# Kernel tuning notes

Measured on AMD Instinct MI355X. Metric: run time of the kernel, lower is better.

Reference implementation:

```python
import jax, jax.numpy as jnp
import numpy as np

N = 50000   # nodes
E = 800000  # edges (avg degree 16)
D = 64      # feature dim (input_dim == hidden_dim == output_dim for num_layer=2)
BN_EPS = 1e-5


def setup_inputs() -> dict:
    key = jax.random.key(0)
    ks = jax.random.split(key, 8)
    def lin_w(k, fan_in, fan_out):
        return jax.random.normal(k, (fan_in, fan_out), jnp.float32) / np.sqrt(fan_in).astype(np.float32)
    inp = {
        "x": jax.random.normal(ks[0], (N, D), jnp.float32),
        "edge_index": jax.random.randint(ks[1], (2, E), 0, N),
    }
    ki = 2
    for l in range(2):
        for s in ("a", "b"):
            inp[f"w{l}{s}"] = lin_w(ks[ki], D, D)
            inp[f"b{l}{s}"] = jnp.zeros((D,), jnp.float32)
            inp[f"g{l}{s}"] = jnp.ones((D,), jnp.float32)   # BN gamma
            inp[f"be{l}{s}"] = jnp.zeros((D,), jnp.float32)  # BN beta
            ki += 1
    inp["lin_w"] = lin_w(ks[6], 2 * D, D)  # JK cat of 2 layers -> 2D, final lin -> D
    inp["lin_b"] = jnp.zeros((D,), jnp.float32)
    return inp


def _bn(h, g, b):
    # BatchNorm1d in training mode: batch statistics over the node axis
    m = h.mean(axis=0)
    v = h.var(axis=0)
    return (h - m) * jax.lax.rsqrt(v + BN_EPS) * g + b


def _gin(h, src, dst, w1, b1, g1, be1, w2, b2, g2, be2):
    # GINConv with eps=0: (1+eps)*x_i + sum_{j->i} x_j, then MLP(Lin-BN-ReLU-Lin-BN-ReLU)
    agg = jax.ops.segment_sum(h[src], dst, num_segments=N) + h
    h = jax.nn.relu(_bn(agg @ w1 + b1, g1, be1))
    return jax.nn.relu(_bn(h @ w2 + b2, g2, be2))


def reference(x, edge_index, w0a, b0a, g0a, be0a, w0b, b0b, g0b, be0b,
              w1a, b1a, g1a, be1a, w1b, b1b, g1b, be1b, lin_w, lin_b):
    src, dst = edge_index[0], edge_index[1]
    h1 = _gin(x, src, dst, w0a, b0a, g0a, be0a, w0b, b0b, g0b, be0b)
    h2 = _gin(h1, src, dst, w1a, b1a, g1a, be1a, w1b, b1b, g1b, be1b)
    # JumpingKnowledge 'cat' over the conv outputs (res[1:]), then final linear
    return jnp.concatenate([h1, h2], axis=1) @ lin_w + lin_b
```

## Files before the change

kernel.cpp:

```cpp
#include <hip/hip_runtime.h>
#include <hip/hip_bf16.h>

#define NN 50000
#define NE 800000
#define BN_EPS 1e-5f
#define CHUNK 4096
#define NCH 196
#define NBK 196

typedef __attribute__((ext_vector_type(4))) float f32x4;
typedef __attribute__((ext_vector_type(8))) short s16x8;
typedef __attribute__((ext_vector_type(4))) short s16x4;

__device__ __forceinline__ float bf2f(__hip_bfloat16 v) { return __bfloat162float(v); }
__device__ __forceinline__ short f2bs(float v) {
    __hip_bfloat16 b = __float2bfloat16(v);
    return __builtin_bit_cast(short, b);
}

__global__ void prep_k(const int* __restrict__ dst, int* __restrict__ part,
                       const float* __restrict__ x, __hip_bfloat16* __restrict__ Xb,
                       const float* __restrict__ w0a, const float* __restrict__ w0b,
                       const float* __restrict__ w1a, const float* __restrict__ w1b,
                       const float* __restrict__ lw,
                       short* __restrict__ Wt0a, short* __restrict__ Wt0b,
                       short* __restrict__ Wt1a, short* __restrict__ Wt1b,
                       short* __restrict__ Wtf) {
    int b = blockIdx.x, t = threadIdx.x;
    if (b < NCH) {
        __shared__ int c[256];
        c[t] = 0;
        __syncthreads();
        int base = b * CHUNK;
        int n = NE - base; if (n > CHUNK) n = CHUNK;
        for (int i = t; i < n; i += 256) atomicAdd(&c[dst[base + i] >> 8], 1);
        __syncthreads();
        part[b * 256 + t] = c[t];
    } else if (b < 196 + 3125) {
        int i = (b - 196) * 256 + t;
        if (i < NN * 16) {
            f32x4 v = *(const f32x4*)(x + (size_t)i * 4);
            s16x4 ov;
            #pragma unroll
            for (int j = 0; j < 4; j++) ov[j] = f2bs(v[j]);
            *(s16x4*)((short*)Xb + (size_t)i * 4) = ov;
        }
    } else {
        int wb = b - 3321;
        if (wb < 4) {
            const float* W = wb == 0 ? w0a : wb == 1 ? w0b : wb == 2 ? w1a : w1b;
            short* Wt = wb == 0 ? Wt0a : wb == 1 ? Wt0b : wb == 2 ? Wt1a : Wt1b;
            for (int e = t; e < 4096; e += 256) {
                int k = e >> 6, n = e & 63;
                Wt[n * 64 + k] = f2bs(W[e]);
            }
        } else {
            for (int e = t; e < 8192; e += 256) {
                int k = e >> 6, n = e & 63;
                Wtf[n * 128 + k] = f2bs(lw[e]);
            }
        }
    }
}

__global__ void bscan_k(const int* __restrict__ part, int* __restrict__ bbase,
                        int* __restrict__ bres, int* __restrict__ off,
                        float* __restrict__ sums) {
    __shared__ int s[256];
    int t = threadIdx.x;
    int v = 0;
    for (int c = 0; c < NCH; c++) v += part[c * 256 + t];
    s[t] = v;
    __syncthreads();
    for (int d = 1; d < 256; d <<= 1) {
        int u = (t >= d) ? s[t - d] : 0;
        __syncthreads();
        s[t] += u;
        __syncthreads();
    }
    int ex = s[t] - v;
    bbase[t] = ex;
    bres[t] = ex;
    if (t == 0) { bbase[256] = NE; off[NN] = NE; }
    sums[t] = 0.f; sums[256 + t] = 0.f;
}

__global__ void bscatter_k(const int* __restrict__ src, const int* __restrict__ dst,
                           int* __restrict__ bres, int* __restrict__ ebuf) {
    __shared__ int cnt[256], loff[256], lcur[256], gst[256], sc[256];
    __shared__ int packed[CHUNK];
    int t = threadIdx.x;
    cnt[t] = 0;
    __syncthreads();
    int base = blockIdx.x * CHUNK;
    int n = NE - base; if (n > CHUNK) n = CHUNK;
    for (int i = t; i < n; i += 256) atomicAdd(&cnt[dst[base + i] >> 8], 1);
    __syncthreads();
    sc[t] = cnt[t];
    __syncthreads();
    for (int d = 1; d < 256; d <<= 1) {
        int u = (t >= d) ? sc[t - d] : 0;
        __syncthreads();
        sc[t] += u;
        __syncthreads();
    }
    loff[t] = sc[t] - cnt[t];
    lcur[t] = loff[t];
    __syncthreads();
    for (int i = t; i < n; i += 256) {
        int d = dst[base + i];
        int b = d >> 8;
        int p = atomicAdd(&lcur[b], 1);
        packed[p] = src[base + i] | ((d & 255) << 16) | (b << 24);
    }
    __syncthreads();
    if (cnt[t]) gst[t] = atomicAdd(&bres[t], cnt[t]);
    __syncthreads();
    for (int i = t; i < n; i += 256) {
        int v = packed[i];
        int b = (v >> 24) & 255;
        ebuf[gst[b] + i - loff[b]] = v & 0xFFFFFF;
    }
}

__global__ void csr_k(const int* __restrict__ bbase, const int* __restrict__ ebuf,
                      int* __restrict__ off, int* __restrict__ adj) {
    __shared__ int cnt[256], loff[256], lcur[256], sc[256];
    int b = blockIdx.x, t = threadIdx.x;
    int s0 = bbase[b], s1 = bbase[b + 1];
    int n = s1 - s0;
    cnt[t] = 0;
    __syncthreads();
    for (int i = t; i < n; i += 256) atomicAdd(&cnt[(ebuf[s0 + i] >> 16) & 255], 1);
    __syncthreads();
    sc[t] = cnt[t];
    __syncthreads();
    for (int d = 1; d < 256; d <<= 1) {
        int u = (t >= d) ? sc[t - d] : 0;
        __syncthreads();
        sc[t] += u;
        __syncthreads();
    }
    loff[t] = sc[t] - cnt[t];
    lcur[t] = loff[t];
    int node = b * 256 + t;
    if (node < NN) off[node] = s0 + loff[t];
    __syncthreads();
    for (int i = t; i < n; i += 256) {
        int v = ebuf[s0 + i];
        int p = atomicAdd(&lcur[(v >> 16) & 255], 1);
        adj[s0 + p] = v & 0xFFFF;
    }
}

__global__ void gather_k(const __hip_bfloat16* __restrict__ X,
                         const int* __restrict__ off, const int* __restrict__ adj,
                         __hip_bfloat16* __restrict__ AGG) {
    int node = blockIdx.x * 4 + (threadIdx.x >> 6);
    int lane = threadIdx.x & 63;
    if (node >= NN) return;
    float acc = bf2f(X[(size_t)node * 64 + lane]);
    int s = off[node], e = off[node + 1];
    int p = s;
    for (; p + 8 <= e; p += 8) {
        int j0 = adj[p + 0], j1 = adj[p + 1], j2 = adj[p + 2], j3 = adj[p + 3];
        int j4 = adj[p + 4], j5 = adj[p + 5], j6 = adj[p + 6], j7 = adj[p + 7];
        float v0 = bf2f(X[(size_t)j0 * 64 + lane]);
        float v1 = bf2f(X[(size_t)j1 * 64 + lane]);
        float v2 = bf2f(X[(size_t)j2 * 64 + lane]);
        float v3 = bf2f(X[(size_t)j3 * 64 + lane]);
        float v4 = bf2f(X[(size_t)j4 * 64 + lane]);
        float v5 = bf2f(X[(size_t)j5 * 64 + lane]);
        float v6 = bf2f(X[(size_t)j6 * 64 + lane]);
        float v7 = bf2f(X[(size_t)j7 * 64 + lane]);
        acc += ((v0 + v1) + (v2 + v3)) + ((v4 + v5) + (v6 + v7));
    }
    if (p + 4 <= e) {
        int j0 = adj[p + 0], j1 = adj[p + 1], j2 = adj[p + 2], j3 = adj[p + 3];
        float v0 = bf2f(X[(size_t)j0 * 64 + lane]);
        float v1 = bf2f(X[(size_t)j1 * 64 + lane]);
        float v2 = bf2f(X[(size_t)j2 * 64 + lane]);
        float v3 = bf2f(X[(size_t)j3 * 64 + lane]);
        acc += (v0 + v1) + (v2 + v3);
        p += 4;
    }
    for (; p < e; p++) acc += bf2f(X[(size_t)adj[p] * 64 + lane]);
    AGG[(size_t)node * 64 + lane] = __float2bfloat16(acc);
}


__global__ void gemm_a_k(const __hip_bfloat16* __restrict__ Ab,
                         const short* __restrict__ Wt,
                         const float* __restrict__ bias,
                         float* __restrict__ T,
                         float* __restrict__ sums) {
    __shared__ float lsum[64], lssq[64];
    int tid = threadIdx.x;
    if (tid < 64) { lsum[tid] = 0.f; lssq[tid] = 0.f; }
    __syncthreads();
    int wv = tid >> 6, L = tid & 63;
    int m = L & 15, quad = L >> 4;
    int wrow = blockIdx.x * 64 + wv * 16;
    int arow = wrow + m;
    if (arow >= NN) arow = NN - 1;
    const short* Ap = (const short*)Ab;
    s16x8 a0 = *(const s16x8*)(Ap + (size_t)arow * 64 + quad * 8);
    s16x8 a1 = *(const s16x8*)(Ap + (size_t)arow * 64 + 32 + quad * 8);
    f32x4 acc[4];
    #pragma unroll
    for (int nt = 0; nt < 4; nt++) {
        int n = nt * 16 + m;
        s16x8 b0 = *(const s16x8*)(Wt + n * 64 + quad * 8);
        s16x8 b1 = *(const s16x8*)(Wt + n * 64 + 32 + quad * 8);
        acc[nt] = (f32x4){0.f, 0.f, 0.f, 0.f};
        acc[nt] = __builtin_amdgcn_mfma_f32_16x16x32_bf16(a0, b0, acc[nt], 0, 0, 0);
        acc[nt] = __builtin_amdgcn_mfma_f32_16x16x32_bf16(a1, b1, acc[nt], 0, 0, 0);
    }
    #pragma unroll
    for (int nt = 0; nt < 4; nt++) {
        int col = nt * 16 + m;
        float bv = bias[col];
        float ps = 0.f, pq = 0.f;
        #pragma unroll
        for (int r = 0; r < 4; r++) {
            int orow = wrow + quad * 4 + r;
            if (orow < NN) {
                float v = acc[nt][r] + bv;
                T[(size_t)orow * 64 + col] = v;
                ps += v;
                pq += v * v;
            }
        }
        atomicAdd(&lsum[col], ps);
        atomicAdd(&lssq[col], pq);
    }
    __syncthreads();
    if (tid < 64) {
        atomicAdd(&sums[tid], lsum[tid]);
        atomicAdd(&sums[64 + tid], lssq[tid]);
    }
}

__global__ void gemm_bn_k(const float* __restrict__ Tin,
                          const float* __restrict__ stats,
                          const float* __restrict__ g, const float* __restrict__ be,
                          const short* __restrict__ Wt,
                          const float* __restrict__ bias,
                          float* __restrict__ T,
                          float* __restrict__ sums) {
    __shared__ float sc[64], sh[64], lsum[64], lssq[64];
    int tid = threadIdx.x;
    if (tid < 64) {
        float mm = stats[tid] * (1.0f / NN);
        float var = stats[64 + tid] * (1.0f / NN) - mm * mm;
        if (var < 0.f) var = 0.f;
        float s = g[tid] * rsqrtf(var + BN_EPS);
        sc[tid] = s;
        sh[tid] = be[tid] - mm * s;
        lsum[tid] = 0.f; lssq[tid] = 0.f;
    }
    __syncthreads();
    int wv = tid >> 6, L = tid & 63;
    int m = L & 15, quad = L >> 4;
    int wrow = blockIdx.x * 64 + wv * 16;
    int arow = wrow + m;
    if (arow >= NN) arow = NN - 1;
    f32x4 t0 = *(const f32x4*)(Tin + (size_t)arow * 64 + quad * 8);
    f32x4 t1 = *(const f32x4*)(Tin + (size_t)arow * 64 + quad * 8 + 4);
    f32x4 t2 = *(const f32x4*)(Tin + (size_t)arow * 64 + 32 + quad * 8);
    f32x4 t3 = *(const f32x4*)(Tin + (size_t)arow * 64 + 32 + quad * 8 + 4);
    s16x8 a0, a1;
    #pragma unroll
    for (int j = 0; j < 4; j++) {
        int k0 = quad * 8 + j, k1 = quad * 8 + 4 + j;
        float u0 = t0[j] * sc[k0] + sh[k0]; a0[j]     = f2bs(u0 > 0.f ? u0 : 0.f);
        float u1 = t1[j] * sc[k1] + sh[k1]; a0[4 + j] = f2bs(u1 > 0.f ? u1 : 0.f);
        float u2 = t2[j] * sc[32 + k0] + sh[32 + k0]; a1[j]     = f2bs(u2 > 0.f ? u2 : 0.f);
        float u3 = t3[j] * sc[32 + k1] + sh[32 + k1]; a1[4 + j] = f2bs(u3 > 0.f ? u3 : 0.f);
    }
    f32x4 acc[4];
    #pragma unroll
    for (int nt = 0; nt < 4; nt++) {
        int n = nt * 16 + m;
        s16x8 b0 = *(const s16x8*)(Wt + n * 64 + quad * 8);
        s16x8 b1 = *(const s16x8*)(Wt + n * 64 + 32 + quad * 8);
        acc[nt] = (f32x4){0.f, 0.f, 0.f, 0.f};
        acc[nt] = __builtin_amdgcn_mfma_f32_16x16x32_bf16(a0, b0, acc[nt], 0, 0, 0);
        acc[nt] = __builtin_amdgcn_mfma_f32_16x16x32_bf16(a1, b1, acc[nt], 0, 0, 0);
    }
    #pragma unroll
    for (int nt = 0; nt < 4; nt++) {
        int col = nt * 16 + m;
        float bv = bias[col];
        float ps = 0.f, pq = 0.f;
        #pragma unroll
        for (int r = 0; r < 4; r++) {
            int orow = wrow + quad * 4 + r;
            if (orow < NN) {
                float v = acc[nt][r] + bv;
                T[(size_t)orow * 64 + col] = v;
                ps += v;
                pq += v * v;
            }
        }
        atomicAdd(&lsum[col], ps);
        atomicAdd(&lssq[col], pq);
    }
    __syncthreads();
    if (tid < 64) {
        atomicAdd(&sums[tid], lsum[tid]);
        atomicAdd(&sums[64 + tid], lssq[tid]);
    }
}

__global__ void bn_k(const float* __restrict__ T, const float* __restrict__ sums,
                     const float* __restrict__ g, const float* __restrict__ be,
                     __hip_bfloat16* __restrict__ Hb) {
    __shared__ float sc[64], sh[64];
    int tid = threadIdx.x;
    if (tid < 64) {
        float m = sums[tid] * (1.0f / NN);
        float var = sums[64 + tid] * (1.0f / NN) - m * m;
        if (var < 0.f) var = 0.f;
        float s = g[tid] * rsqrtf(var + BN_EPS);
        sc[tid] = s;
        sh[tid] = be[tid] - m * s;
    }
    __syncthreads();
    int i = blockIdx.x * 256 + tid;
    if (i < NN * 16) {
        int row = i >> 4, f = (i & 15) * 4;
        f32x4 v = *(const f32x4*)(T + (size_t)row * 64 + f);
        s16x4 ub;
        #pragma unroll
        for (int j = 0; j < 4; j++) {
            float w = v[j] * sc[f + j] + sh[f + j];
            ub[j] = f2bs(w > 0.f ? w : 0.f);
        }
        *(s16x4*)((short*)Hb + (size_t)row * 64 + f) = ub;
    }
}

__global__ void gemm_fin_k(const __hip_bfloat16* __restrict__ H1b,
                           const float* __restrict__ T2,
                           const float* __restrict__ stats,
                           const float* __restrict__ g, const float* __restrict__ be,
                           const short* __restrict__ Wtf,
                           const float* __restrict__ bias,
                           float* __restrict__ O) {
    __shared__ float sc[64], sh[64];
    int tid = threadIdx.x;
    if (tid < 64) {
        float mm = stats[tid] * (1.0f / NN);
        float var = stats[64 + tid] * (1.0f / NN) - mm * mm;
        if (var < 0.f) var = 0.f;
        float s = g[tid] * rsqrtf(var + BN_EPS);
        sc[tid] = s;
        sh[tid] = be[tid] - mm * s;
    }
    __syncthreads();
    int wv = tid >> 6, L = tid & 63;
    int m = L & 15, quad = L >> 4;
    int wrow = blockIdx.x * 64 + wv * 16;
    int arow = wrow + m;
    if (arow >= NN) arow = NN - 1;
    const short* Hp = (const short*)H1b;
    s16x8 a0 = *(const s16x8*)(Hp + (size_t)arow * 64 + quad * 8);
    s16x8 a1 = *(const s16x8*)(Hp + (size_t)arow * 64 + 32 + quad * 8);
    f32x4 t0 = *(const f32x4*)(T2 + (size_t)arow * 64 + quad * 8);
    f32x4 t1 = *(const f32x4*)(T2 + (size_t)arow * 64 + quad * 8 + 4);
    f32x4 t2 = *(const f32x4*)(T2 + (size_t)arow * 64 + 32 + quad * 8);
    f32x4 t3 = *(const f32x4*)(T2 + (size_t)arow * 64 + 32 + quad * 8 + 4);
    s16x8 a2, a3;
    #pragma unroll
    for (int j = 0; j < 4; j++) {
        int k0 = quad * 8 + j, k1 = quad * 8 + 4 + j;
        float u0 = t0[j] * sc[k0] + sh[k0]; a2[j]     = f2bs(u0 > 0.f ? u0 : 0.f);
        float u1 = t1[j] * sc[k1] + sh[k1]; a2[4 + j] = f2bs(u1 > 0.f ? u1 : 0.f);
        float u2 = t2[j] * sc[32 + k0] + sh[32 + k0]; a3[j]     = f2bs(u2 > 0.f ? u2 : 0.f);
        float u3 = t3[j] * sc[32 + k1] + sh[32 + k1]; a3[4 + j] = f2bs(u3 > 0.f ? u3 : 0.f);
    }
    f32x4 acc[4];
    #pragma unroll
    for (int nt = 0; nt < 4; nt++) {
        int n = nt * 16 + m;
        s16x8 b0 = *(const s16x8*)(Wtf + n * 128 + quad * 8);
        s16x8 b1 = *(const s16x8*)(Wtf + n * 128 + 32 + quad * 8);
        s16x8 b2 = *(const s16x8*)(Wtf + n * 128 + 64 + quad * 8);
        s16x8 b3 = *(const s16x8*)(Wtf + n * 128 + 96 + quad * 8);
        acc[nt] = (f32x4){0.f, 0.f, 0.f, 0.f};
        acc[nt] = __builtin_amdgcn_mfma_f32_16x16x32_bf16(a0, b0, acc[nt], 0, 0, 0);
        acc[nt] = __builtin_amdgcn_mfma_f32_16x16x32_bf16(a1, b1, acc[nt], 0, 0, 0);
        acc[nt] = __builtin_amdgcn_mfma_f32_16x16x32_bf16(a2, b2, acc[nt], 0, 0, 0);
        acc[nt] = __builtin_amdgcn_mfma_f32_16x16x32_bf16(a3, b3, acc[nt], 0, 0, 0);
    }
    #pragma unroll
    for (int nt = 0; nt < 4; nt++) {
        int col = nt * 16 + m;
        float bv = bias[col];
        #pragma unroll
        for (int r = 0; r < 4; r++) {
            int orow = wrow + quad * 4 + r;
            if (orow < NN) O[(size_t)orow * 64 + col] = acc[nt][r] + bv;
        }
    }
}

extern "C" void kernel_launch(void* const* d_in, const int* in_sizes, int n_in,
                              void* d_out, int out_size, void* d_ws, size_t ws_size,
                              hipStream_t stream) {
    const float* x   = (const float*)d_in[0];
    const int*   ei  = (const int*)d_in[1];
    const float* w0a = (const float*)d_in[2];
    const float* b0a = (const float*)d_in[3];
    const float* g0a = (const float*)d_in[4];
    const float* be0a= (const float*)d_in[5];
    const float* w0b = (const float*)d_in[6];
    const float* b0b = (const float*)d_in[7];
    const float* g0b = (const float*)d_in[8];
    const float* be0b= (const float*)d_in[9];
    const float* w1a = (const float*)d_in[10];
    const float* b1a = (const float*)d_in[11];
    const float* g1a = (const float*)d_in[12];
    const float* be1a= (const float*)d_in[13];
    const float* w1b = (const float*)d_in[14];
    const float* b1b = (const float*)d_in[15];
    const float* g1b = (const float*)d_in[16];
    const float* be1b= (const float*)d_in[17];
    const float* lw  = (const float*)d_in[18];
    const float* lb  = (const float*)d_in[19];
    float* out = (float*)d_out;
    (void)in_sizes; (void)n_in; (void)out_size; (void)ws_size;

    char* wsb = (char*)d_ws;
    size_t o = 0;
    auto alloc = [&](size_t bytes) -> char* {
        char* p = wsb + o;
        o += (bytes + 255) & ~(size_t)255;
        return p;
    };
    int* part = (int*)alloc(NCH * 256 * 4);
    float* sums = (float*)alloc(512 * 4);
    int* bbase = (int*)alloc(257 * 4);
    int* bres = (int*)alloc(256 * 4);
    int* off = (int*)alloc((NN + 1) * 4);
    int* adj = (int*)alloc(NE * 4);
    int* ebuf = (int*)alloc(NE * 4);
    __hip_bfloat16* Xb   = (__hip_bfloat16*)alloc((size_t)NN * 64 * 2);
    __hip_bfloat16* AGGb = (__hip_bfloat16*)alloc((size_t)NN * 64 * 2);
    __hip_bfloat16* HCb  = (__hip_bfloat16*)alloc((size_t)NN * 64 * 2);
    float* T  = (float*)alloc((size_t)NN * 64 * 4);
    float* T2 = (float*)alloc((size_t)NN * 64 * 4);
    short* Wt0a = (short*)alloc(4096 * 2);
    short* Wt0b = (short*)alloc(4096 * 2);
    short* Wt1a = (short*)alloc(4096 * 2);
    short* Wt1b = (short*)alloc(4096 * 2);
    short* Wtf  = (short*)alloc(8192 * 2);

    const int* src = ei;
    const int* dst = ei + NE;

    prep_k<<<3326, 256, 0, stream>>>(dst, part, x, Xb, w0a, w0b, w1a, w1b, lw,
                                     Wt0a, Wt0b, Wt1a, Wt1b, Wtf);
    bscan_k<<<1, 256, 0, stream>>>(part, bbase, bres, off, sums);
    bscatter_k<<<NCH, 256, 0, stream>>>(src, dst, bres, ebuf);
    csr_k<<<NBK, 256, 0, stream>>>(bbase, ebuf, off, adj);

    const int ggrid = NN / 4;
    const int mgrid = (NN + 63) / 64;
    const int agrid = (NN * 16 + 255) / 256;

    gather_k<<<ggrid, 256, 0, stream>>>(Xb, off, adj, AGGb);
    gemm_a_k<<<mgrid, 256, 0, stream>>>(AGGb, Wt0a, b0a, T, sums + 0);
    gemm_bn_k<<<mgrid, 256, 0, stream>>>(T, sums + 0, g0a, be0a, Wt0b, b0b, T2, sums + 128);
    bn_k<<<agrid, 256, 0, stream>>>(T2, sums + 128, g0b, be0b, HCb);

    gather_k<<<ggrid, 256, 0, stream>>>(HCb, off, adj, AGGb);
    gemm_a_k<<<mgrid, 256, 0, stream>>>(AGGb, Wt1a, b1a, T, sums + 256);
    gemm_bn_k<<<mgrid, 256, 0, stream>>>(T, sums + 256, g1a, be1a, Wt1b, b1b, T2, sums + 384);

    gemm_fin_k<<<mgrid, 256, 0, stream>>>(HCb, T2, sums + 384, g1b, be1b, Wtf, lb, out);
}
```

Before: 348.3 us.

## Fuse neighbor gather into first GEMM using MFMA-layout row accumulation

Merges the CSR neighbor-sum kernel into the first linear layer's MFMA kernel. Each lane now gathers two 16-byte chunks of neighbor rows in exactly the fragment layout the MFMA needs, so the bf16 aggregate no longer round-trips through global memory and one launch per layer is removed. The trade-off is that each wave now handles only 16 nodes, four lanes share a row, and the gather is less unrolled (4 neighbors instead of 8). This could reduce memory-level parallelism or occupancy compared with the dedicated gather kernel.

```diff
diff --git a/kernel.cpp b/kernel.cpp
--- a/kernel.cpp
+++ b/kernel.cpp
@@ -13,6 +13,10 @@
 typedef __attribute__((ext_vector_type(4))) short s16x4;
 
 __device__ __forceinline__ float bf2f(__hip_bfloat16 v) { return __bfloat162float(v); }
+__device__ __forceinline__ float bs2f(short v) {
+    unsigned u = ((unsigned)(unsigned short)v) << 16;
+    return __builtin_bit_cast(float, u);
+}
 __device__ __forceinline__ short f2bs(float v) {
     __hip_bfloat16 b = __float2bfloat16(v);
     return __builtin_bit_cast(short, b);
@@ -153,59 +157,60 @@
     }
 }
 
-__global__ void gather_k(const __hip_bfloat16* __restrict__ X,
-                         const int* __restrict__ off, const int* __restrict__ adj,
-                         __hip_bfloat16* __restrict__ AGG) {
-    int node = blockIdx.x * 4 + (threadIdx.x >> 6);
-    int lane = threadIdx.x & 63;
-    if (node >= NN) return;
-    float acc = bf2f(X[(size_t)node * 64 + lane]);
+__global__ void ggemm_k(const __hip_bfloat16* __restrict__ X,
+                        const int* __restrict__ off, const int* __restrict__ adj,
+                        const short* __restrict__ Wt,
+                        const float* __restrict__ bias,
+                        float* __restrict__ T,
+                        float* __restrict__ sums) {
+    __shared__ float lsum[64], lssq[64];
+    int t = threadIdx.x;
+    if (t < 64) { lsum[t] = 0.f; lssq[t] = 0.f; }
+    __syncthreads();
+    int wv = t >> 6, L = t & 63;
+    int m = L & 15, quad = L >> 4;
+    int wrow = blockIdx.x * 64 + wv * 16;
+    int node = wrow + m;
+    if (node >= NN) node = NN - 1;
+    const short* Xp = (const short*)X;
+
+    const short* rp = Xp + (size_t)node * 64 + quad * 8;
+    s16x8 sl = *(const s16x8*)rp;
+    s16x8 sh = *(const s16x8*)(rp + 32);
+    float aL[8], aH[8];
+    #pragma unroll
+    for (int j = 0; j < 8; j++) { aL[j] = bs2f(sl[j]); aH[j] = bs2f(sh[j]); }
+
     int s = off[node], e = off[node + 1];
     int p = s;
-    for (; p + 8 <= e; p += 8) {
-        int j0 = adj[p + 0], j1 = adj[p + 1], j2 = adj[p + 2], j3 = adj[p + 3];
-        int j4 = adj[p + 4], j5 = adj[p + 5], j6 = adj[p + 6], j7 = adj[p + 7];
-        float v0 = bf2f(X[(size_t)j0 * 64 + lane]);
-        float v1 = bf2f(X[(size_t)j1 * 64 + lane]);
-        float v2 = bf2f(X[(size_t)j2 * 64 + lane]);
-        float v3 = bf2f(X[(size_t)j3 * 64 + lane]);
-        float v4 = bf2f(X[(size_t)j4 * 64 + lane]);
-        float v5 = bf2f(X[(size_t)j5 * 64 + lane]);
-        float v6 = bf2f(X[(size_t)j6 * 64 + lane]);
-        float v7 = bf2f(X[(size_t)j7 * 64 + lane]);
-        acc += ((v0 + v1) + (v2 + v3)) + ((v4 + v5) + (v6 + v7));
-    }
-    if (p + 4 <= e) {
-        int j0 = adj[p + 0], j1 = adj[p + 1], j2 = adj[p + 2], j3 = adj[p + 3];
-        float v0 = bf2f(X[(size_t)j0 * 64 + lane]);
-        float v1 = bf2f(X[(size_t)j1 * 64 + lane]);
-        float v2 = bf2f(X[(size_t)j2 * 64 + lane]);
-        float v3 = bf2f(X[(size_t)j3 * 64 + lane]);
-        acc += (v0 + v1) + (v2 + v3);
-        p += 4;
-    }
-    for (; p < e; p++) acc += bf2f(X[(size_t)adj[p] * 64 + lane]);
-    AGG[(size_t)node * 64 + lane] = __float2bfloat16(acc);
-}
-
-
-__global__ void gemm_a_k(const __hip_bfloat16* __restrict__ Ab,
-                         const short* __restrict__ Wt,
-                         const float* __restrict__ bias,
-                         float* __restrict__ T,
-                         float* __restrict__ sums) {
-    __shared__ float lsum[64], lssq[64];
-    int tid = threadIdx.x;
-    if (tid < 64) { lsum[tid] = 0.f; lssq[tid] = 0.f; }
-    __syncthreads();
-    int wv = tid >> 6, L = tid & 63;
-    int m = L & 15, quad = L >> 4;
-    int wrow = blockIdx.x * 64 + wv * 16;
-    int arow = wrow + m;
-    if (arow >= NN) arow = NN - 1;
-    const short* Ap = (const short*)Ab;
-    s16x8 a0 = *(const s16x8*)(Ap + (size_t)arow * 64 + quad * 8);
-    s16x8 a1 = *(const s16x8*)(Ap + (size_t)arow * 64 + 32 + quad * 8);
+    for (; p + 4 <= e; p += 4) {
+        int j0 = adj[p], j1 = adj[p + 1], j2 = adj[p + 2], j3 = adj[p + 3];
+        const short* r0 = Xp + (size_t)j0 * 64 + quad * 8;
+        const short* r1 = Xp + (size_t)j1 * 64 + quad * 8;
+        const short* r2 = Xp + (size_t)j2 * 64 + quad * 8;
+        const short* r3 = Xp + (size_t)j3 * 64 + quad * 8;
+        s16x8 v0 = *(const s16x8*)r0, w0 = *(const s16x8*)(r0 + 32);
+        s16x8 v1 = *(const s16x8*)r1, w1 = *(const s16x8*)(r1 + 32);
+        s16x8 v2 = *(const s16x8*)r2, w2 = *(const s16x8*)(r2 + 32);
+        s16x8 v3 = *(const s16x8*)r3, w3 = *(const s16x8*)(r3 + 32);
+        #pragma unroll
+        for (int j = 0; j < 8; j++) {
+            aL[j] += (bs2f(v0[j]) + bs2f(v1[j])) + (bs2f(v2[j]) + bs2f(v3[j]));
+            aH[j] += (bs2f(w0[j]) + bs2f(w1[j])) + (bs2f(w2[j]) + bs2f(w3[j]));
+        }
+    }
+    for (; p < e; p++) {
+        int j0 = adj[p];
+        const short* r0 = Xp + (size_t)j0 * 64 + quad * 8;
+        s16x8 v0 = *(const s16x8*)r0, w0 = *(const s16x8*)(r0 + 32);
+        #pragma unroll
+        for (int j = 0; j < 8; j++) { aL[j] += bs2f(v0[j]); aH[j] += bs2f(w0[j]); }
+    }
+
+    s16x8 a0, a1;
+    #pragma unroll
+    for (int j = 0; j < 8; j++) { a0[j] = f2bs(aL[j]); a1[j] = f2bs(aH[j]); }
+
     f32x4 acc[4];
     #pragma unroll
     for (int nt = 0; nt < 4; nt++) {
@@ -235,9 +240,9 @@
         atomicAdd(&lssq[col], pq);
     }
     __syncthreads();
-    if (tid < 64) {
-        atomicAdd(&sums[tid], lsum[tid]);
-        atomicAdd(&sums[64 + tid], lssq[tid]);
+    if (t < 64) {
+        atomicAdd(&sums[t], lsum[t]);
+        atomicAdd(&sums[64 + t], lssq[t]);
     }
 }
 
@@ -446,9 +451,8 @@
     int* off = (int*)alloc((NN + 1) * 4);
     int* adj = (int*)alloc(NE * 4);
     int* ebuf = (int*)alloc(NE * 4);
-    __hip_bfloat16* Xb   = (__hip_bfloat16*)alloc((size_t)NN * 64 * 2);
-    __hip_bfloat16* AGGb = (__hip_bfloat16*)alloc((size_t)NN * 64 * 2);
-    __hip_bfloat16* HCb  = (__hip_bfloat16*)alloc((size_t)NN * 64 * 2);
+    __hip_bfloat16* Xb  = (__hip_bfloat16*)alloc((size_t)NN * 64 * 2);
+    __hip_bfloat16* HCb = (__hip_bfloat16*)alloc((size_t)NN * 64 * 2);
     float* T  = (float*)alloc((size_t)NN * 64 * 4);
     float* T2 = (float*)alloc((size_t)NN * 64 * 4);
     short* Wt0a = (short*)alloc(4096 * 2);
@@ -466,17 +470,14 @@
     bscatter_k<<<NCH, 256, 0, stream>>>(src, dst, bres, ebuf);
     csr_k<<<NBK, 256, 0, stream>>>(bbase, ebuf, off, adj);
 
-    const int ggrid = NN / 4;
     const int mgrid = (NN + 63) / 64;
     const int agrid = (NN * 16 + 255) / 256;
 
-    gather_k<<<ggrid, 256, 0, stream>>>(Xb, off, adj, AGGb);
-    gemm_a_k<<<mgrid, 256, 0, stream>>>(AGGb, Wt0a, b0a, T, sums + 0);
+    ggemm_k<<<mgrid, 256, 0, stream>>>(Xb, off, adj, Wt0a, b0a, T, sums + 0);
     gemm_bn_k<<<mgrid, 256, 0, stream>>>(T, sums + 0, g0a, be0a, Wt0b, b0b, T2, sums + 128);
     bn_k<<<agrid, 256, 0, stream>>>(T2, sums + 128, g0b, be0b, HCb);
 
-    gather_k<<<ggrid, 256, 0, stream>>>(HCb, off, adj, AGGb);
-    gemm_a_k<<<mgrid, 256, 0, stream>>>(AGGb, Wt1a, b1a, T, sums + 256);
+    ggemm_k<<<mgrid, 256, 0, stream>>>(HCb, off, adj, Wt1a, b1a, T, sums + 256);
     gemm_bn_k<<<mgrid, 256, 0, stream>>>(T, sums + 256, g1a, be1a, Wt1b, b1b, T2, sums + 384);
 
     gemm_fin_k<<<mgrid, 256, 0, stream>>>(HCb, T2, sums + 384, g1b, be1b, Wtf, lb, out);
```

New measurement: 322.0 us. -7.6%, faster.
